# Optimization experiments

Hardware: AMD Instinct MI355X
Metric: run time of the kernel (lower is better)

The kernel has to match this reference:

```python
import jax, jax.numpy as jnp
import numpy as np
from jax import lax

PI = float(np.pi)
K_TOP = 128
N_BINS = 64

def _normalize(x, axis, eps=1e-12):
    n = jnp.sqrt(jnp.sum(x * x, axis=axis, keepdims=True))
    return x / jnp.maximum(n, eps)

def _conv(x, w, b):
    y = lax.conv_general_dilated(x, w, (1, 1), 'SAME',
                                 dimension_numbers=('NCHW', 'OIHW', 'NCHW'))
    return y + b[None, :, None, None]

def _maxpool2(x):
    return lax.reduce_window(x, -jnp.inf, lax.max, (1, 1, 2, 2), (1, 1, 2, 2), 'VALID')

def setup_inputs() -> dict:
    key = jax.random.key(0)
    ks = jax.random.split(key, 12)
    B, C, H, W = 16, 1, 512, 512
    PD, NPT = 128, 64
    fc_in = NPT + 64 * 4 * 4 + 3  # 1091
    def lin_init(k, fan_in, shape):
        bound = 1.0 / np.sqrt(fan_in)
        return jax.random.uniform(k, shape, jnp.float32, -bound, bound)
    return {
        'image': jax.random.normal(ks[0], (B, C, H, W), jnp.float32),
        'pattern_receptors': jax.random.normal(ks[1], (NPT, PD), jnp.float32) * 0.1,
        'conv1_w': lin_init(ks[2], 2 * 9, (32, 2, 3, 3)),
        'conv1_b': lin_init(ks[3], 2 * 9, (32,)),
        'conv2_w': lin_init(ks[4], 32 * 9, (64, 32, 3, 3)),
        'conv2_b': lin_init(ks[5], 32 * 9, (64,)),
        'fc1_w': lin_init(ks[6], fc_in, (512, fc_in)),
        'fc1_b': lin_init(ks[7], fc_in, (512,)),
        'fc2_w': lin_init(ks[8], 512, (PD, 512)),
        'fc2_b': lin_init(ks[9], 512, (PD,)),
        'ln_g': jnp.ones((PD,), jnp.float32),
        'ln_b': jnp.zeros((PD,), jnp.float32),
    }

def reference(image, pattern_receptors, conv1_w, conv1_b, conv2_w, conv2_b,
              fc1_w, fc1_b, fc2_w, fc2_b, ln_g, ln_b):
    B, C, H, W = image.shape
    # ---- frequency domain ----
    freq = jnp.fft.fft2(image, axes=(2, 3))
    magnitude = jnp.abs(freq)
    phase = jnp.angle(freq)
    # ---- pattern matching (topk of FFT magnitude vs receptor library) ----
    flat_mag = magnitude.reshape(B, C, -1)
    dom, _ = lax.top_k(flat_mag, K_TOP)          # [B, C, 128]
    dom = dom.reshape(B, -1)                     # [B, C*128]
    sims = jnp.matmul(_normalize(dom, 1), _normalize(pattern_receptors, 1).T)  # [B, 64]
    # ---- spatial path (original detaches via numpy roundtrip) ----
    img = lax.stop_gradient(image)
    gy = jnp.gradient(img, axis=2)
    gx = jnp.gradient(img, axis=3)
    gmag = jnp.sqrt(gx * gx + gy * gy)
    gori = jnp.arctan2(gy, gx)
    spat_in = jnp.stack([gmag, gori], axis=2).reshape(B, 2 * C, H, W)
    h = jax.nn.relu(_conv(spat_in, conv1_w, conv1_b))
    h = _maxpool2(h)                             # [B,32,H/2,W/2]
    h = jax.nn.relu(_conv(h, conv2_w, conv2_b))  # [B,64,H/2,W/2]
    Hp, Wp = h.shape[2], h.shape[3]
    h = h.reshape(B, 64, 4, Hp // 4, 4, Wp // 4).mean(axis=(3, 5))  # adaptive avg 4x4
    spatial = h.reshape(B, -1)                   # [B, 1024]
    # ---- phase statistics ----
    pf = phase.reshape(B, -1)
    p_mean = jnp.mean(pf, axis=1)
    p_std = jnp.std(pf, axis=1, ddof=1)
    bins = jnp.clip(jnp.floor((pf + PI) / (2 * PI) * N_BINS), 0, N_BINS - 1).astype(jnp.int32)
    hist = jnp.zeros((B, N_BINS), jnp.float32).at[jnp.arange(B)[:, None], bins].add(1.0)
    hist = hist / jnp.sum(hist, axis=1, keepdims=True)
    p_ent = -jnp.sum(hist * jnp.log(hist + 1e-10), axis=1)
    phase_feats = jnp.stack([p_mean, p_std, p_ent], axis=1)  # [B, 3]
    # ---- fuse: MLP + LayerNorm ----
    combined = jnp.concatenate([sims, spatial, phase_feats], axis=1)  # [B, 1091]
    z = jax.nn.relu(combined @ fc1_w.T + fc1_b)
    z = z @ fc2_w.T + fc2_b
    mu = jnp.mean(z, axis=-1, keepdims=True)
    var = jnp.var(z, axis=-1, keepdims=True)
    holo = (z - mu) / jnp.sqrt(var + 1e-5) * ln_g + ln_b
    return sims, spatial, phase_feats, holo
```

## Files before the change

### kernel.cpp

```cpp
#include <hip/hip_runtime.h>
#include <hip/hip_fp16.h>
#include <math.h>


#define PI_F 3.14159274f
#define TWO_PI_F 6.28318548f

typedef _Float16 half8 __attribute__((ext_vector_type(8)));
typedef _Float16 h2 __attribute__((ext_vector_type(2)));
typedef float floatx4 __attribute__((ext_vector_type(4)));

#define OFF_BIG   8388608
#define OFF_SMALL 25165824
#define NBIN 2048

__global__ void __launch_bounds__(256) init_kernel(float* __restrict__ zp,
                                                   float2* __restrict__ tw,
                                                   const float* __restrict__ w2,
                                                   const float* __restrict__ w1,
                                                   _Float16* __restrict__ wrep,
                                                   _Float16* __restrict__ w1r) {
    int idx = blockIdx.x * 256 + threadIdx.x;
    if (idx < 82992) zp[idx] = 0.0f;
    if (idx < 512) {
        if (idx == 0) tw[0] = make_float2(1.f, 0.f);
        else {
            int h = 31 - __clz(idx);
            int H = 1 << h;
            float sn, cs;
            sincosf(-PI_F * (float)(idx - H) / (float)H, &sn, &cs);
            tw[idx] = make_float2(cs, sn);
        }
    }
    if (idx < 18432) {
        int j = idx & 7;
        int lane = (idx >> 3) & 63;
        int nt = (idx >> 9) & 3;
        int tap = idx >> 11;
        int oc = nt * 16 + (lane & 15);
        int ic = (lane >> 4) * 8 + j;
        wrep[idx] = (_Float16)w2[(oc * 32 + ic) * 9 + tap];
    }
    if (idx < 1024) {
        int j = idx & 7;
        int lane = (idx >> 3) & 63;
        int nt = idx >> 9;
        int oc = 2 * (lane & 15) + nt;
        int k = (lane >> 4) * 8 + j;
        _Float16 v = (_Float16)0.f;
        if (k < 18) {
            int tap = k >> 1, ch = k & 1;
            v = (_Float16)w1[oc * 18 + ch * 9 + tap];
        }
        w1r[idx] = v;
    }
}

__global__ void __launch_bounds__(256) fft_rows2(const float* __restrict__ img,
                                                 const float2* __restrict__ twg,
                                                 h2* __restrict__ rowhf) {
    __shared__ float2 s[512];
    __shared__ float2 tw[512];
    const int t = threadIdx.x;
    const long long rbase = (long long)blockIdx.x * 1024;
    const float* x0 = img + rbase;
    const float* x1 = x0 + 512;

    for (int i = t; i < 512; i += 256) tw[i] = twg[i];
    for (int i = t; i < 512; i += 256) s[i] = make_float2(x0[i], x1[i]);
    __syncthreads();
#pragma unroll
    for (int st = 9; st >= 1; --st) {
        const int half = 1 << (st - 1);
        const int pos = t & (half - 1);
        const int grp = t >> (st - 1);
        const int i1 = (grp << st) + pos;
        const int i2 = i1 + half;
        float2 w = tw[half + pos];
        float2 a = s[i1], b = s[i2];
        float dx = a.x - b.x, dy = a.y - b.y;
        s[i1] = make_float2(a.x + b.x, a.y + b.y);
        s[i2] = make_float2(dx * w.x - dy * w.y, dx * w.y + dy * w.x);
        __syncthreads();
    }
    for (int i = t; i < 512; i += 256) {
        int k = __brev((unsigned)i) >> 23;
        int kp = (512 - k) & 511;
        int jp = __brev((unsigned)kp) >> 23;
        float2 Z = s[i], Zp = s[jp];
        rowhf[rbase + i]       = h2{(_Float16)(0.5f * (Z.x + Zp.x)),
                                    (_Float16)(0.5f * (Z.y - Zp.y))};
        rowhf[rbase + 512 + i] = h2{(_Float16)(0.5f * (Z.y + Zp.y)),
                                    (_Float16)(-0.5f * (Z.x - Zp.x))};
    }
}

#define FCOLS 16
__global__ void __launch_bounds__(512) fft_cols(const h2* __restrict__ rowhf,
                                                const float2* __restrict__ twg,
                                                _Float16* __restrict__ magT,
                                                float* __restrict__ psum,
                                                float* __restrict__ psumsq,
                                                unsigned* __restrict__ phist,
                                                unsigned* __restrict__ mhist) {
    __shared__ h2 sh[FCOLS * 512];
    __shared__ float2 tw[512];
    __shared__ unsigned ph[64];
    __shared__ unsigned mh[NBIN];
    __shared__ float red[16];
    const int t = threadIdx.x;
    const int b = blockIdx.x >> 5;
    const int x0 = (blockIdx.x & 31) * FCOLS;

    for (int i = t; i < 512; i += 512) tw[i] = twg[i];
    if (t < 64) ph[t] = 0u;
    for (int i = t; i < NBIN; i += 512) mh[i] = 0u;
    for (int idx = t; idx < FCOLS * 512; idx += 512) {
        int y = idx >> 4, c = idx & 15;
        sh[c * 512 + y] = rowhf[((size_t)(b * 512 + y)) * 512 + x0 + c];
    }
    __syncthreads();

    const int c = t >> 5;
    const int j = t & 31;
    float2 v[16];
#pragma unroll
    for (int r = 0; r < 16; ++r) {
        h2 hv = sh[c * 512 + j + 32 * r];
        v[r] = make_float2((float)hv[0], (float)hv[1]);
    }
#pragma unroll
    for (int r = 0; r < 8; ++r) {
        float2 w = tw[256 + j + 32 * r];
        float2 a = v[r], bb = v[r + 8];
        float dx = a.x - bb.x, dy = a.y - bb.y;
        v[r]     = make_float2(a.x + bb.x, a.y + bb.y);
        v[r + 8] = make_float2(dx * w.x - dy * w.y, dx * w.y + dy * w.x);
    }
#pragma unroll
    for (int g = 0; g < 2; ++g)
#pragma unroll
        for (int rr = 0; rr < 4; ++rr) {
            int r = g * 8 + rr;
            float2 w = tw[128 + j + 32 * rr];
            float2 a = v[r], bb = v[r + 4];
            float dx = a.x - bb.x, dy = a.y - bb.y;
            v[r]     = make_float2(a.x + bb.x, a.y + bb.y);
            v[r + 4] = make_float2(dx * w.x - dy * w.y, dx * w.y + dy * w.x);
        }
#pragma unroll
    for (int g = 0; g < 4; ++g)
#pragma unroll
        for (int rr = 0; rr < 2; ++rr) {
            int r = g * 4 + rr;
            float2 w = tw[64 + j + 32 * rr];
            float2 a = v[r], bb = v[r + 2];
            float dx = a.x - bb.x, dy = a.y - bb.y;
            v[r]     = make_float2(a.x + bb.x, a.y + bb.y);
            v[r + 2] = make_float2(dx * w.x - dy * w.y, dx * w.y + dy * w.x);
        }
    {
        float2 w = tw[32 + j];
#pragma unroll
        for (int g = 0; g < 8; ++g) {
            int r = g * 2;
            float2 a = v[r], bb = v[r + 1];
            float dx = a.x - bb.x, dy = a.y - bb.y;
            v[r]     = make_float2(a.x + bb.x, a.y + bb.y);
            v[r + 1] = make_float2(dx * w.x - dy * w.y, dx * w.y + dy * w.x);
        }
    }
#pragma unroll
    for (int hs = 4; hs >= 0; --hs) {
        const int h = 1 << hs;
        float2 w = tw[h + (j & (h - 1))];
        const bool upper = (j & h) != 0;
#pragma unroll
        for (int r = 0; r < 16; ++r) {
            float ox = __shfl_xor(v[r].x, h);
            float oy = __shfl_xor(v[r].y, h);
            float sx = v[r].x + ox, sy = v[r].y + oy;
            float dx = ox - v[r].x, dy = oy - v[r].y;
            float tx = dx * w.x - dy * w.y, ty = dx * w.y + dy * w.x;
            v[r].x = upper ? tx : sx;
            v[r].y = upper ? ty : sy;
        }
    }

    float lsum = 0.f, lsq = 0.f;
    _Float16* mcol = magT + ((size_t)(b * 512 + x0 + c)) * 512;
#pragma unroll
    for (int r = 0; r < 16; ++r) {
        float mag = sqrtf(v[r].x * v[r].x + v[r].y * v[r].y);
        union { _Float16 h; unsigned short u; } cvt;
        cvt.h = (_Float16)mag;
        mcol[j + 32 * r] = cvt.h;
        atomicAdd(&mh[min((unsigned)(cvt.u >> 4), (unsigned)(NBIN - 1))], 1u);
        float phv = atan2f(v[r].y, v[r].x);
        lsum += phv;
        lsq += phv * phv;
        int bin = min(max((int)floorf((phv + PI_F) / TWO_PI_F * 64.0f), 0), 63);
        atomicAdd(&ph[bin], 1u);
    }
    for (int off = 32; off > 0; off >>= 1) {
        lsum += __shfl_down(lsum, off);
        lsq  += __shfl_down(lsq, off);
    }
    if ((t & 63) == 0) { red[t >> 6] = lsum; red[8 + (t >> 6)] = lsq; }
    __syncthreads();
    if (t == 0) {
        float s = 0.f, q = 0.f;
        for (int i = 0; i < 8; ++i) { s += red[i]; q += red[8 + i]; }
        atomicAdd(psum + b, s);
        atomicAdd(psumsq + b, q);
    }
    if (t < 64 && ph[t]) atomicAdd(&phist[b * 64 + t], ph[t]);
    for (int i = t; i < NBIN; i += 512)
        if (mh[i]) atomicAdd(&mhist[b * NBIN + i], mh[i]);
}

__global__ void __launch_bounds__(256) thresh_kernel(const unsigned* __restrict__ mhist,
                                                     int* __restrict__ selbin) {
    __shared__ unsigned csum[256];
    const int b = blockIdx.x, t = threadIdx.x;
    unsigned s = 0;
    for (int i = 0; i < NBIN / 256; ++i) s += mhist[b * NBIN + t * (NBIN / 256) + i];
    csum[t] = s;
    __syncthreads();
    if (t == 0) {
        unsigned acc = 0; int chunk = 0;
        for (int i = 255; i >= 0; --i) {
            acc += csum[i];
            if (acc >= 128u) { chunk = i; break; }
        }
        unsigned acc2 = acc - csum[chunk];
        int tb = chunk * (NBIN / 256);
        for (int i = chunk * (NBIN / 256) + (NBIN / 256) - 1; i >= chunk * (NBIN / 256); --i) {
            acc2 += mhist[b * NBIN + i];
            if (acc2 >= 128u) { tb = i; break; }
        }
        selbin[b] = tb;
    }
}

#define TK_CAP 4096
__global__ void __launch_bounds__(256) collect_kernel(const _Float16* __restrict__ magT,
                                                      const int* __restrict__ selbin,
                                                      float* __restrict__ cand,
                                                      unsigned* __restrict__ ccnt) {
    const int blk = blockIdx.x;
    const int b = blk >> 4, chunk = blk & 15;
    const unsigned tb = (unsigned)selbin[b];
    const uint4* m = (const uint4*)(magT + (size_t)b * 262144 + chunk * 16384);
    float* cb = cand + b * TK_CAP;
    for (int i = threadIdx.x; i < 2048; i += 256) {
        uint4 v4 = m[i];
        unsigned vv[4] = {v4.x, v4.y, v4.z, v4.w};
#pragma unroll
        for (int j = 0; j < 4; ++j) {
#pragma unroll
            for (int k = 0; k < 2; ++k) {
                unsigned short ub = (k == 0) ? (unsigned short)(vv[j] & 0xFFFFu)
                                             : (unsigned short)(vv[j] >> 16);
                if ((unsigned)(ub >> 4) >= tb) {
                    unsigned p = atomicAdd(&ccnt[b], 1u);
                    if (p < TK_CAP) {
                        union { unsigned short u; _Float16 h; } c2;
                        c2.u = ub;
                        cb[p] = (float)c2.h;
                    }
                }
            }
        }
    }
}

__global__ void __launch_bounds__(1024) sort_kernel(const float* __restrict__ cand,
                                                    const unsigned* __restrict__ ccnt,
                                                    float* __restrict__ dom) {
    __shared__ float c[TK_CAP];
    const int b = blockIdx.x, t = threadIdx.x;
    const unsigned n = min(ccnt[b], (unsigned)TK_CAP);
    int P = 256;
    while (P < (int)n) P <<= 1;
    for (int i = t; i < P; i += 1024) c[i] = (i < (int)n) ? cand[b * TK_CAP + i] : -1.0f;
    __syncthreads();
    for (int k = 2; k <= P; k <<= 1) {
        for (int j = k >> 1; j > 0; j >>= 1) {
            for (int i = t; i < P; i += 1024) {
                int ixj = i ^ j;
                if (ixj > i) {
                    float a = c[i], d = c[ixj];
                    bool up = ((i & k) == 0);
                    if (up ? (a < d) : (a > d)) { c[i] = d; c[ixj] = a; }
                }
            }
            __syncthreads();
        }
    }
    if (t < 128) dom[b * 128 + t] = c[t];
}

__global__ void __launch_bounds__(256) sims_kernel(const float* __restrict__ dom,
                                                   const float* __restrict__ rec,
                                                   float* __restrict__ comb,
                                                   float* __restrict__ dout) {
    __shared__ float sd[16 * 128];
    __shared__ float sr[64 * 128];
    __shared__ float scale[80];
    const int t = threadIdx.x;
    for (int i = t; i < 2048; i += 256) sd[i] = dom[i];
    for (int i = t; i < 8192; i += 256) sr[i] = rec[i];
    __syncthreads();
    if (t < 80) {
        const float* base = (t < 16) ? (sd + t * 128) : (sr + (t - 16) * 128);
        float s = 0.f;
        for (int k = 0; k < 128; ++k) s += base[k] * base[k];
        scale[t] = 1.0f / fmaxf(sqrtf(s), 1e-12f);
    }
    __syncthreads();
    for (int o = t; o < 1024; o += 256) {
        int b = o >> 6, p = o & 63;
        const float* dv = sd + b * 128;
        const float* rv = sr + p * 128;
        float s = 0.f;
        for (int k = 0; k < 128; ++k) s += dv[k] * rv[k];
        float val = s * scale[b] * scale[16 + p];
        dout[b * 64 + p] = val;
        comb[b * 1091 + p] = val;
    }
}

__global__ void __launch_bounds__(256) grad_conv1_mfma(const float* __restrict__ img,
                                                       const half8* __restrict__ w1r,
                                                       const float* __restrict__ c1b,
                                                       _Float16* __restrict__ h1) {
    __shared__ float simg[36 * 37];
    __shared__ _Float16 sgrad[(34 * 36 + 1) * 2];
    const int blk = blockIdx.x;
    const int b = blk >> 8;
    const int tr = blk & 255;
    const int TY = (tr >> 4) * 32, TX = (tr & 15) * 32;
    const int t = threadIdx.x;
    const float* im = img + (long long)b * 262144;

    for (int idx = t; idx < 1296; idx += 256) {
        int iy = idx / 36, ix = idx - iy * 36;
        int gy = min(max(TY - 2 + iy, 0), 511);
        int gx = min(max(TX - 2 + ix, 0), 511);
        simg[iy * 37 + ix] = im[gy * 512 + gx];
    }
    if (t == 0) { sgrad[2448] = (_Float16)0.f; sgrad[2449] = (_Float16)0.f; }
    __syncthreads();

    for (int idx = t; idx < 1156; idx += 256) {
        int ly = idx / 34, lx = idx - ly * 34;
        int gy = TY - 1 + ly, gx = TX - 1 + lx;
        float up = simg[ly * 37 + lx + 1];
        float dn = simg[(ly + 2) * 37 + lx + 1];
        float lf = simg[(ly + 1) * 37 + lx];
        float rt = simg[(ly + 1) * 37 + lx + 2];
        float fy = (gy <= 0 || gy >= 511) ? 1.f : 0.5f;
        float fx = (gx <= 0 || gx >= 511) ? 1.f : 0.5f;
        float gyv = (dn - up) * fy, gxv = (rt - lf) * fx;
        bool inside = ((unsigned)gy < 512u) && ((unsigned)gx < 512u);
        float mag = inside ? sqrtf(gxv * gxv + gyv * gyv) : 0.f;
        float ori = inside ? atan2f(gyv, gxv) : 0.f;
        int p = (ly * 36 + lx) * 2;
        sgrad[p] = (_Float16)mag;
        sgrad[p + 1] = (_Float16)ori;
    }
    __syncthreads();

    const int w = t >> 6, lane = t & 63;
    const int q = lane >> 4, m = lane & 15;
    const int oc0 = 2 * m, oc1 = 2 * m + 1;
    const float bias0 = c1b[oc0], bias1 = c1b[oc1];
    half8 Bf0 = w1r[lane], Bf1 = w1r[64 + lane];
    const unsigned* gp = (const unsigned*)sgrad;
    const int ZP = 1224;

    const int sy = (m >> 1) & 1, sx = m & 1, dqx = m >> 2;

#pragma unroll 4
    for (int i = 0; i < 16; ++i) {
        const int mt = w * 16 + i;
        const int qy = mt >> 2, qxg = mt & 3;
        const int py = 2 * qy + sy;
        const int px = 2 * (qxg * 4 + dqx) + sx;
        const int base = py * 36 + px;

        int o0 = (q == 0) ? base      : (q == 1) ? base + 37 : (q == 2) ? base + 74 : ZP;
        int o1 = (q == 0) ? base + 1  : (q == 1) ? base + 38 : ZP;
        int o2 = (q == 0) ? base + 2  : (q == 1) ? base + 72 : ZP;
        int o3 = (q == 0) ? base + 36 : (q == 1) ? base + 73 : ZP;

        union { unsigned u[4]; half8 h; } Af;
        Af.u[0] = gp[o0]; Af.u[1] = gp[o1]; Af.u[2] = gp[o2]; Af.u[3] = gp[o3];

        floatx4 acc0 = {bias0, bias0, bias0, bias0};
        floatx4 acc1 = {bias1, bias1, bias1, bias1};
        acc0 = __builtin_amdgcn_mfma_f32_16x16x32_f16(Af.h, Bf0, acc0, 0, 0, 0);
        acc1 = __builtin_amdgcn_mfma_f32_16x16x32_f16(Af.h, Bf1, acc1, 0, 0, 0);

        float v0 = fmaxf(fmaxf(acc0[0], acc0[1]), fmaxf(acc0[2], acc0[3]));
        float v1 = fmaxf(fmaxf(acc1[0], acc1[1]), fmaxf(acc1[2], acc1[3]));
        v0 = fmaxf(v0, 0.f);
        v1 = fmaxf(v1, 0.f);

        const int PY = (TY >> 1) + qy;
        const int PX = (TX >> 1) + qxg * 4 + q;
        _Float16* dst = h1 + (((size_t)(b * 256 + PY)) * 256 + PX) * 32;
        *(h2*)(dst + oc0) = h2{(_Float16)v0, (_Float16)v1};
    }
}

__global__ void __launch_bounds__(256) conv2_mfma(const _Float16* __restrict__ h1,
                                                  const _Float16* __restrict__ wrep,
                                                  const float* __restrict__ c2b,
                                                  float* __restrict__ sacc) {
    __shared__ _Float16 tile[18 * 34 * 32];
    __shared__ float lsum[64];
    const int blk = blockIdx.x;
    const int b  = blk >> 7;
    const int yt = (blk >> 3) & 15;
    const int xt = blk & 7;
    const int y0 = yt * 16, x0 = xt * 32;
    const int t = threadIdx.x;
    if (t < 64) lsum[t] = 0.f;

    for (int c = t; c < 18 * 136; c += 256) {
        int row = c / 136;
        int chunk = c - row * 136;
        int gy = y0 - 1 + row;
        int px = chunk >> 2;
        int gx = x0 - 1 + px;
        floatx4 v = {0.f, 0.f, 0.f, 0.f};
        if ((unsigned)gy < 256u && (unsigned)gx < 256u)
            v = *(const floatx4*)(h1 + (((size_t)(b * 256 + gy)) * 256 + gx) * 32 + (chunk & 3) * 8);
        *(floatx4*)(tile + (row * 34 + px) * 32 + (chunk & 3) * 8) = v;
    }
    __syncthreads();

    const int w = t >> 6, lane = t & 63;
    const int q = lane >> 4, ln15 = lane & 15;
    float bias[4];
#pragma unroll
    for (int nt = 0; nt < 4; ++nt) bias[nt] = c2b[nt * 16 + ln15];
    float partial[4] = {0.f, 0.f, 0.f, 0.f};

#pragma unroll 1
    for (int gr = 0; gr < 2; ++gr) {
        floatx4 acc[4][4];
#pragma unroll
        for (int mt = 0; mt < 4; ++mt)
#pragma unroll
            for (int nt = 0; nt < 4; ++nt)
                acc[mt][nt] = floatx4{bias[nt], bias[nt], bias[nt], bias[nt]};

        const _Float16* ab = tile + (((w * 4 + gr * 2) * 34) + ln15) * 32 + q * 8;
        const _Float16* wk = wrep + lane * 8;

#pragma unroll 1
        for (int ky = 0; ky < 3; ++ky) {
#pragma unroll
            for (int kx = 0; kx < 3; ++kx) {
                half8 Bf[4];
#pragma unroll
                for (int nt = 0; nt < 4; ++nt)
                    Bf[nt] = *(const half8*)(wk + (kx * 4 + nt) * 512);
#pragma unroll
                for (int mt = 0; mt < 4; ++mt) {
                    half8 Af = *(const half8*)(ab + (mt >> 1) * 1088 + (mt & 1) * 512 + kx * 32);
#pragma unroll
                    for (int nt = 0; nt < 4; ++nt)
                        acc[mt][nt] = __builtin_amdgcn_mfma_f32_16x16x32_f16(Af, Bf[nt], acc[mt][nt], 0, 0, 0);
                }
            }
            ab += 34 * 32;
            wk += 3 * 2048;
        }

#pragma unroll
        for (int mt = 0; mt < 4; ++mt)
#pragma unroll
            for (int nt = 0; nt < 4; ++nt)
#pragma unroll
                for (int rg = 0; rg < 4; ++rg)
                    partial[nt] += fmaxf(acc[mt][nt][rg], 0.f);
    }

#pragma unroll
    for (int nt = 0; nt < 4; ++nt) {
        float v = partial[nt];
        v += __shfl_xor(v, 16);
        v += __shfl_xor(v, 32);
        if (lane < 16) atomicAdd(&lsum[nt * 16 + ln15], v);
    }
    __syncthreads();
    const int cell = (yt >> 2) * 4 + (xt >> 1);
    if (t < 64) atomicAdd(&sacc[(((b << 6) + t) << 4) + cell], lsum[t]);
}

__global__ void __launch_bounds__(256) finalize_kernel(const float* __restrict__ sacc,
                                                       const float* __restrict__ psum,
                                                       const float* __restrict__ psumsq,
                                                       const unsigned* __restrict__ phist,
                                                       float* __restrict__ comb,
                                                       float* __restrict__ dout) {
    if (blockIdx.x < 64) {
        int idx = blockIdx.x * 256 + threadIdx.x;
        int b = idx >> 10, j = idx & 1023;
        float v = sacc[idx] * (1.0f / 4096.0f);
        dout[1024 + idx] = v;
        comb[b * 1091 + 64 + j] = v;
    } else {
        int t = threadIdx.x;
        if (t < 16) {
            const float N = 262144.f;
            float s = psum[t];
            float mean = s / N;
            float var = (psumsq[t] - s * s / N) / (N - 1.f);
            float sd = sqrtf(fmaxf(var, 0.f));
            float ent = 0.f;
            for (int i = 0; i < 64; ++i) {
                float p = (float)phist[t * 64 + i] / N;
                ent -= p * logf(p + 1e-10f);
            }
            dout[17408 + t * 3 + 0] = mean;
            dout[17408 + t * 3 + 1] = sd;
            dout[17408 + t * 3 + 2] = ent;
            float* cb = comb + t * 1091 + 1088;
            cb[0] = mean; cb[1] = sd; cb[2] = ent;
        }
    }
}

__global__ void __launch_bounds__(256) fc1_kernel(const float* __restrict__ comb,
                                                  const float* __restrict__ W1,
                                                  const float* __restrict__ B1,
                                                  float* __restrict__ out1) {
    const int wid = blockIdx.x * 4 + (threadIdx.x >> 6);
    const int lane = threadIdx.x & 63;
    const int b = wid >> 9, o = wid & 511;
    const float* w = W1 + (size_t)o * 1091;
    const float* c = comb + b * 1091;
    float acc = 0.f;
#pragma unroll 4
    for (int i = 0; i < 17; ++i) {
        int k = i * 64 + lane;
        acc += w[k] * c[k];
    }
    if (lane < 3) acc += w[1088 + lane] * c[1088 + lane];
#pragma unroll
    for (int off = 32; off > 0; off >>= 1) acc += __shfl_down(acc, off);
    if (lane == 0) out1[b * 512 + o] = fmaxf(acc + B1[o], 0.f);
}

__global__ void __launch_bounds__(256) fc2_kernel(const float* __restrict__ out1,
                                                  const float* __restrict__ W2,
                                                  const float* __restrict__ B2,
                                                  float* __restrict__ z) {
    const int wid = blockIdx.x * 4 + (threadIdx.x >> 6);
    const int lane = threadIdx.x & 63;
    const int b = wid >> 7, o = wid & 127;
    const float* w = W2 + (size_t)o * 512;
    const float* c = out1 + b * 512;
    float acc = 0.f;
#pragma unroll
    for (int i = 0; i < 8; ++i) {
        int k = i * 64 + lane;
        acc += w[k] * c[k];
    }
#pragma unroll
    for (int off = 32; off > 0; off >>= 1) acc += __shfl_down(acc, off);
    if (lane == 0) z[b * 128 + o] = acc + B2[o];
}

__global__ void __launch_bounds__(128) ln_kernel(const float* __restrict__ z,
                                                 const float* __restrict__ g,
                                                 const float* __restrict__ beta,
                                                 float* __restrict__ dout) {
    __shared__ float red[4];
    const int b = blockIdx.x, t = threadIdx.x;
    float acc = z[b * 128 + t];
    float s = acc;
    for (int off = 32; off > 0; off >>= 1) s += __shfl_down(s, off);
    if ((t & 63) == 0) red[t >> 6] = s;
    __syncthreads();
    float mu = (red[0] + red[1]) * (1.0f / 128.0f);
    float d = acc - mu;
    float q = d * d;
    for (int off = 32; off > 0; off >>= 1) q += __shfl_down(q, off);
    if ((t & 63) == 0) red[2 + (t >> 6)] = q;
    __syncthreads();
    float var = (red[2] + red[3]) * (1.0f / 128.0f);
    dout[17456 + b * 128 + t] = d / sqrtf(var + 1e-5f) * g[t] + beta[t];
}

extern "C" void kernel_launch(void* const* d_in, const int* in_sizes, int n_in,
                              void* d_out, int out_size, void* d_ws, size_t ws_size,
                              hipStream_t stream) {
    const float* img = (const float*)d_in[0];
    const float* rec = (const float*)d_in[1];
    const float* w1  = (const float*)d_in[2];
    const float* c1b = (const float*)d_in[3];
    const float* w2  = (const float*)d_in[4];
    const float* c2b = (const float*)d_in[5];
    const float* fw1 = (const float*)d_in[6];
    const float* fb1 = (const float*)d_in[7];
    const float* fw2 = (const float*)d_in[8];
    const float* fb2 = (const float*)d_in[9];
    const float* lng = (const float*)d_in[10];
    const float* lnb = (const float*)d_in[11];
    float* out = (float*)d_out;

    float* ws = (float*)d_ws;
    h2* rowhf       = (h2*)ws;
    _Float16* magT  = (_Float16*)(ws + OFF_BIG);
    _Float16* h1    = (_Float16*)(ws + OFF_BIG);
    float* small_  = ws + OFF_SMALL;
    float* sacc    = small_;
    float* psum    = small_ + 16384;
    float* psumsq  = small_ + 16400;
    unsigned* phist = (unsigned*)(small_ + 16416);
    unsigned* mhist = (unsigned*)(small_ + 17440);
    unsigned* ccnt  = (unsigned*)(small_ + 82976);
    int* selbin    = (int*)(small_ + 82992);
    float* dom     = small_ + 83008;
    float* comb    = small_ + 85056;
    float* out1    = small_ + 102512;
    _Float16* wrep = (_Float16*)(small_ + 110704);
    float2* twg    = (float2*)(small_ + 119920);
    float* cand    = small_ + 120944;
    float* zbuf    = cand;
    _Float16* w1r  = (_Float16*)(small_ + 186480);

    init_kernel<<<325, 256, 0, stream>>>(sacc, twg, w2, w1, wrep, w1r);
    fft_rows2<<<4096, 256, 0, stream>>>(img, twg, rowhf);
    fft_cols<<<512, 512, 0, stream>>>(rowhf, twg, magT, psum, psumsq, phist, mhist);
    thresh_kernel<<<16, 256, 0, stream>>>(mhist, selbin);
    collect_kernel<<<256, 256, 0, stream>>>(magT, selbin, cand, ccnt);
    sort_kernel<<<16, 1024, 0, stream>>>(cand, ccnt, dom);
    sims_kernel<<<1, 256, 0, stream>>>(dom, rec, comb, out);
    grad_conv1_mfma<<<4096, 256, 0, stream>>>(img, (const half8*)w1r, c1b, h1);
    conv2_mfma<<<2048, 256, 0, stream>>>(h1, wrep, c2b, sacc);
    finalize_kernel<<<65, 256, 0, stream>>>(sacc, psum, psumsq, phist, comb, out);
    fc1_kernel<<<2048, 256, 0, stream>>>(comb, fw1, fb1, out1);
    fc2_kernel<<<512, 256, 0, stream>>>(out1, fw2, fb2, zbuf);
    ln_kernel<<<16, 128, 0, stream>>>(zbuf, lng, lnb, out);
}
```

Measured before the change: 279.5 us.

## Fuse column FFT, top-k threshold and candidate collection into cooperative kernel

Replaces the column-FFT, threshold and collect kernels with one cooperative kernel of 256 blocks. Each block processes 32 columns and keeps the fp16 magnitudes in registers. After a grid-wide sync it finds the threshold bin with a shared-memory suffix scan and collects candidates directly, so the magnitude array is never written to or re-read from global memory. The similarity computation moves into the sort kernel, removing a single-block launch. In exchange, each block does two column passes serially, and the grid barrier plus the fixed 256-block grid may limit occupancy.

```diff
diff --git a/kernel.cpp b/kernel.cpp
--- a/kernel.cpp
+++ b/kernel.cpp
@@ -1,6 +1,9 @@
 #include <hip/hip_runtime.h>
 #include <hip/hip_fp16.h>
+#include <hip/hip_cooperative_groups.h>
 #include <math.h>
+
+namespace cg = cooperative_groups;
 
 
 #define PI_F 3.14159274f
@@ -95,113 +98,128 @@
     }
 }
 
-#define FCOLS 16
-__global__ void __launch_bounds__(512) fft_cols(const h2* __restrict__ rowhf,
-                                                const float2* __restrict__ twg,
-                                                _Float16* __restrict__ magT,
-                                                float* __restrict__ psum,
-                                                float* __restrict__ psumsq,
-                                                unsigned* __restrict__ phist,
-                                                unsigned* __restrict__ mhist) {
-    __shared__ h2 sh[FCOLS * 512];
+#define TK_CAP 4096
+__global__ void __launch_bounds__(512) fftcol_coop(const h2* __restrict__ rowhf,
+                                                   const float2* __restrict__ twg,
+                                                   float* __restrict__ psum,
+                                                   float* __restrict__ psumsq,
+                                                   unsigned* __restrict__ phist,
+                                                   unsigned* __restrict__ mhist,
+                                                   float* __restrict__ cand,
+                                                   unsigned* __restrict__ ccnt) {
+    __shared__ h2 sh[16 * 512];
     __shared__ float2 tw[512];
     __shared__ unsigned ph[64];
     __shared__ unsigned mh[NBIN];
     __shared__ float red[16];
+    __shared__ unsigned scanA[512], scanB[512];
+    __shared__ int seltb;
     const int t = threadIdx.x;
-    const int b = blockIdx.x >> 5;
-    const int x0 = (blockIdx.x & 31) * FCOLS;
+    const int b = blockIdx.x >> 4;
+    const int xg = blockIdx.x & 15;
 
     for (int i = t; i < 512; i += 512) tw[i] = twg[i];
     if (t < 64) ph[t] = 0u;
     for (int i = t; i < NBIN; i += 512) mh[i] = 0u;
-    for (int idx = t; idx < FCOLS * 512; idx += 512) {
-        int y = idx >> 4, c = idx & 15;
-        sh[c * 512 + y] = rowhf[((size_t)(b * 512 + y)) * 512 + x0 + c];
-    }
-    __syncthreads();
 
     const int c = t >> 5;
     const int j = t & 31;
-    float2 v[16];
-#pragma unroll
-    for (int r = 0; r < 16; ++r) {
-        h2 hv = sh[c * 512 + j + 32 * r];
-        v[r] = make_float2((float)hv[0], (float)hv[1]);
-    }
-#pragma unroll
-    for (int r = 0; r < 8; ++r) {
-        float2 w = tw[256 + j + 32 * r];
-        float2 a = v[r], bb = v[r + 8];
-        float dx = a.x - bb.x, dy = a.y - bb.y;
-        v[r]     = make_float2(a.x + bb.x, a.y + bb.y);
-        v[r + 8] = make_float2(dx * w.x - dy * w.y, dx * w.y + dy * w.x);
-    }
-#pragma unroll
-    for (int g = 0; g < 2; ++g)
-#pragma unroll
-        for (int rr = 0; rr < 4; ++rr) {
-            int r = g * 8 + rr;
-            float2 w = tw[128 + j + 32 * rr];
-            float2 a = v[r], bb = v[r + 4];
+    float lsum = 0.f, lsq = 0.f;
+    unsigned mgp[16];
+
+#pragma unroll 1
+    for (int cgi = 0; cgi < 2; ++cgi) {
+        const int x0 = xg * 32 + cgi * 16;
+        __syncthreads();
+        for (int idx = t; idx < 16 * 512; idx += 512) {
+            int y = idx >> 4, cc = idx & 15;
+            sh[cc * 512 + y] = rowhf[((size_t)(b * 512 + y)) * 512 + x0 + cc];
+        }
+        __syncthreads();
+
+        float2 v[16];
+#pragma unroll
+        for (int r = 0; r < 16; ++r) {
+            h2 hv = sh[c * 512 + j + 32 * r];
+            v[r] = make_float2((float)hv[0], (float)hv[1]);
+        }
+        __syncthreads();
+
+#pragma unroll
+        for (int r = 0; r < 8; ++r) {
+            float2 w = tw[256 + j + 32 * r];
+            float2 a = v[r], bb = v[r + 8];
             float dx = a.x - bb.x, dy = a.y - bb.y;
             v[r]     = make_float2(a.x + bb.x, a.y + bb.y);
-            v[r + 4] = make_float2(dx * w.x - dy * w.y, dx * w.y + dy * w.x);
-        }
-#pragma unroll
-    for (int g = 0; g < 4; ++g)
-#pragma unroll
-        for (int rr = 0; rr < 2; ++rr) {
-            int r = g * 4 + rr;
-            float2 w = tw[64 + j + 32 * rr];
-            float2 a = v[r], bb = v[r + 2];
-            float dx = a.x - bb.x, dy = a.y - bb.y;
-            v[r]     = make_float2(a.x + bb.x, a.y + bb.y);
-            v[r + 2] = make_float2(dx * w.x - dy * w.y, dx * w.y + dy * w.x);
-        }
-    {
-        float2 w = tw[32 + j];
-#pragma unroll
-        for (int g = 0; g < 8; ++g) {
-            int r = g * 2;
-            float2 a = v[r], bb = v[r + 1];
-            float dx = a.x - bb.x, dy = a.y - bb.y;
-            v[r]     = make_float2(a.x + bb.x, a.y + bb.y);
-            v[r + 1] = make_float2(dx * w.x - dy * w.y, dx * w.y + dy * w.x);
-        }
-    }
-#pragma unroll
-    for (int hs = 4; hs >= 0; --hs) {
-        const int h = 1 << hs;
-        float2 w = tw[h + (j & (h - 1))];
-        const bool upper = (j & h) != 0;
+            v[r + 8] = make_float2(dx * w.x - dy * w.y, dx * w.y + dy * w.x);
+        }
+#pragma unroll
+        for (int g = 0; g < 2; ++g)
+#pragma unroll
+            for (int rr = 0; rr < 4; ++rr) {
+                int r = g * 8 + rr;
+                float2 w = tw[128 + j + 32 * rr];
+                float2 a = v[r], bb = v[r + 4];
+                float dx = a.x - bb.x, dy = a.y - bb.y;
+                v[r]     = make_float2(a.x + bb.x, a.y + bb.y);
+                v[r + 4] = make_float2(dx * w.x - dy * w.y, dx * w.y + dy * w.x);
+            }
+#pragma unroll
+        for (int g = 0; g < 4; ++g)
+#pragma unroll
+            for (int rr = 0; rr < 2; ++rr) {
+                int r = g * 4 + rr;
+                float2 w = tw[64 + j + 32 * rr];
+                float2 a = v[r], bb = v[r + 2];
+                float dx = a.x - bb.x, dy = a.y - bb.y;
+                v[r]     = make_float2(a.x + bb.x, a.y + bb.y);
+                v[r + 2] = make_float2(dx * w.x - dy * w.y, dx * w.y + dy * w.x);
+            }
+        {
+            float2 w = tw[32 + j];
+#pragma unroll
+            for (int g = 0; g < 8; ++g) {
+                int r = g * 2;
+                float2 a = v[r], bb = v[r + 1];
+                float dx = a.x - bb.x, dy = a.y - bb.y;
+                v[r]     = make_float2(a.x + bb.x, a.y + bb.y);
+                v[r + 1] = make_float2(dx * w.x - dy * w.y, dx * w.y + dy * w.x);
+            }
+        }
+#pragma unroll
+        for (int hs = 4; hs >= 0; --hs) {
+            const int h = 1 << hs;
+            float2 w = tw[h + (j & (h - 1))];
+            const bool upper = (j & h) != 0;
+#pragma unroll
+            for (int r = 0; r < 16; ++r) {
+                float ox = __shfl_xor(v[r].x, h);
+                float oy = __shfl_xor(v[r].y, h);
+                float sx = v[r].x + ox, sy = v[r].y + oy;
+                float dx = ox - v[r].x, dy = oy - v[r].y;
+                float tx = dx * w.x - dy * w.y, ty = dx * w.y + dy * w.x;
+                v[r].x = upper ? tx : sx;
+                v[r].y = upper ? ty : sy;
+            }
+        }
+
 #pragma unroll
         for (int r = 0; r < 16; ++r) {
-            float ox = __shfl_xor(v[r].x, h);
-            float oy = __shfl_xor(v[r].y, h);
-            float sx = v[r].x + ox, sy = v[r].y + oy;
-            float dx = ox - v[r].x, dy = oy - v[r].y;
-            float tx = dx * w.x - dy * w.y, ty = dx * w.y + dy * w.x;
-            v[r].x = upper ? tx : sx;
-            v[r].y = upper ? ty : sy;
-        }
-    }
-
-    float lsum = 0.f, lsq = 0.f;
-    _Float16* mcol = magT + ((size_t)(b * 512 + x0 + c)) * 512;
-#pragma unroll
-    for (int r = 0; r < 16; ++r) {
-        float mag = sqrtf(v[r].x * v[r].x + v[r].y * v[r].y);
-        union { _Float16 h; unsigned short u; } cvt;
-        cvt.h = (_Float16)mag;
-        mcol[j + 32 * r] = cvt.h;
-        atomicAdd(&mh[min((unsigned)(cvt.u >> 4), (unsigned)(NBIN - 1))], 1u);
-        float phv = atan2f(v[r].y, v[r].x);
-        lsum += phv;
-        lsq += phv * phv;
-        int bin = min(max((int)floorf((phv + PI_F) / TWO_PI_F * 64.0f), 0), 63);
-        atomicAdd(&ph[bin], 1u);
-    }
+            float mag = sqrtf(v[r].x * v[r].x + v[r].y * v[r].y);
+            union { _Float16 h; unsigned short u; } cvt;
+            cvt.h = (_Float16)mag;
+            int ei = cgi * 16 + r;
+            if (ei & 1) mgp[ei >> 1] |= ((unsigned)cvt.u) << 16;
+            else        mgp[ei >> 1] = (unsigned)cvt.u;
+            atomicAdd(&mh[min((unsigned)(cvt.u >> 4), (unsigned)(NBIN - 1))], 1u);
+            float phv = atan2f(v[r].y, v[r].x);
+            lsum += phv;
+            lsq += phv * phv;
+            int bin = min(max((int)floorf((phv + PI_F) / TWO_PI_F * 64.0f), 0), 63);
+            atomicAdd(&ph[bin], 1u);
+        }
+    }
+
     for (int off = 32; off > 0; off >>= 1) {
         lsum += __shfl_down(lsum, off);
         lsq  += __shfl_down(lsq, off);
@@ -217,58 +235,53 @@
     if (t < 64 && ph[t]) atomicAdd(&phist[b * 64 + t], ph[t]);
     for (int i = t; i < NBIN; i += 512)
         if (mh[i]) atomicAdd(&mhist[b * NBIN + i], mh[i]);
-}
-
-__global__ void __launch_bounds__(256) thresh_kernel(const unsigned* __restrict__ mhist,
-                                                     int* __restrict__ selbin) {
-    __shared__ unsigned csum[256];
-    const int b = blockIdx.x, t = threadIdx.x;
-    unsigned s = 0;
-    for (int i = 0; i < NBIN / 256; ++i) s += mhist[b * NBIN + t * (NBIN / 256) + i];
-    csum[t] = s;
-    __syncthreads();
-    if (t == 0) {
-        unsigned acc = 0; int chunk = 0;
-        for (int i = 255; i >= 0; --i) {
-            acc += csum[i];
-            if (acc >= 128u) { chunk = i; break; }
-        }
-        unsigned acc2 = acc - csum[chunk];
-        int tb = chunk * (NBIN / 256);
-        for (int i = chunk * (NBIN / 256) + (NBIN / 256) - 1; i >= chunk * (NBIN / 256); --i) {
-            acc2 += mhist[b * NBIN + i];
-            if (acc2 >= 128u) { tb = i; break; }
-        }
-        selbin[b] = tb;
-    }
-}
-
-#define TK_CAP 4096
-__global__ void __launch_bounds__(256) collect_kernel(const _Float16* __restrict__ magT,
-                                                      const int* __restrict__ selbin,
-                                                      float* __restrict__ cand,
-                                                      unsigned* __restrict__ ccnt) {
-    const int blk = blockIdx.x;
-    const int b = blk >> 4, chunk = blk & 15;
-    const unsigned tb = (unsigned)selbin[b];
-    const uint4* m = (const uint4*)(magT + (size_t)b * 262144 + chunk * 16384);
+
+    cg::this_grid().sync();
+
+    {
+        unsigned s = 0;
+#pragma unroll
+        for (int i = 0; i < 4; ++i) s += mhist[b * NBIN + t * 4 + i];
+        scanA[t] = s;
+        __syncthreads();
+        unsigned* src = scanA;
+        unsigned* dst = scanB;
+#pragma unroll
+        for (int off = 1; off < 512; off <<= 1) {
+            unsigned val = src[t] + ((t + off < 512) ? src[t + off] : 0u);
+            dst[t] = val;
+            __syncthreads();
+            unsigned* tmp = src; src = dst; dst = tmp;
+            __syncthreads();
+        }
+        unsigned sufNext = (t < 511) ? src[t + 1] : 0u;
+        if (src[t] >= 128u && sufNext < 128u) {
+            unsigned acc = sufNext;
+            int tb = t * 4;
+            for (int i = t * 4 + 3; i >= t * 4; --i) {
+                acc += mhist[b * NBIN + i];
+                if (acc >= 128u) { tb = i; break; }
+            }
+            seltb = tb;
+        }
+        __syncthreads();
+    }
+    const unsigned tb = (unsigned)seltb;
+
     float* cb = cand + b * TK_CAP;
-    for (int i = threadIdx.x; i < 2048; i += 256) {
-        uint4 v4 = m[i];
-        unsigned vv[4] = {v4.x, v4.y, v4.z, v4.w};
-#pragma unroll
-        for (int j = 0; j < 4; ++j) {
-#pragma unroll
-            for (int k = 0; k < 2; ++k) {
-                unsigned short ub = (k == 0) ? (unsigned short)(vv[j] & 0xFFFFu)
-                                             : (unsigned short)(vv[j] >> 16);
-                if ((unsigned)(ub >> 4) >= tb) {
-                    unsigned p = atomicAdd(&ccnt[b], 1u);
-                    if (p < TK_CAP) {
-                        union { unsigned short u; _Float16 h; } c2;
-                        c2.u = ub;
-                        cb[p] = (float)c2.h;
-                    }
+#pragma unroll
+    for (int i = 0; i < 16; ++i) {
+        unsigned vv = mgp[i];
+#pragma unroll
+        for (int k = 0; k < 2; ++k) {
+            unsigned short ub = (k == 0) ? (unsigned short)(vv & 0xFFFFu)
+                                         : (unsigned short)(vv >> 16);
+            if ((unsigned)(ub >> 4) >= tb) {
+                unsigned p = atomicAdd(&ccnt[b], 1u);
+                if (p < TK_CAP) {
+                    union { unsigned short u; _Float16 h; } c2;
+                    c2.u = ub;
+                    cb[p] = (float)c2.h;
                 }
             }
         }
@@ -277,7 +290,9 @@
 
 __global__ void __launch_bounds__(1024) sort_kernel(const float* __restrict__ cand,
                                                     const unsigned* __restrict__ ccnt,
-                                                    float* __restrict__ dom) {
+                                                    const float* __restrict__ rec,
+                                                    float* __restrict__ comb,
+                                                    float* __restrict__ dout) {
     __shared__ float c[TK_CAP];
     const int b = blockIdx.x, t = threadIdx.x;
     const unsigned n = min(ccnt[b], (unsigned)TK_CAP);
@@ -298,36 +313,19 @@
             __syncthreads();
         }
     }
-    if (t < 128) dom[b * 128 + t] = c[t];
-}
-
-__global__ void __launch_bounds__(256) sims_kernel(const float* __restrict__ dom,
-                                                   const float* __restrict__ rec,
-                                                   float* __restrict__ comb,
-                                                   float* __restrict__ dout) {
-    __shared__ float sd[16 * 128];
-    __shared__ float sr[64 * 128];
-    __shared__ float scale[80];
-    const int t = threadIdx.x;
-    for (int i = t; i < 2048; i += 256) sd[i] = dom[i];
-    for (int i = t; i < 8192; i += 256) sr[i] = rec[i];
-    __syncthreads();
-    if (t < 80) {
-        const float* base = (t < 16) ? (sd + t * 128) : (sr + (t - 16) * 128);
-        float s = 0.f;
-        for (int k = 0; k < 128; ++k) s += base[k] * base[k];
-        scale[t] = 1.0f / fmaxf(sqrtf(s), 1e-12f);
-    }
-    __syncthreads();
-    for (int o = t; o < 1024; o += 256) {
-        int b = o >> 6, p = o & 63;
-        const float* dv = sd + b * 128;
-        const float* rv = sr + p * 128;
-        float s = 0.f;
-        for (int k = 0; k < 128; ++k) s += dv[k] * rv[k];
-        float val = s * scale[b] * scale[16 + p];
-        dout[b * 64 + p] = val;
-        comb[b * 1091 + p] = val;
+    if (t < 64) {
+        float dn = 0.f;
+        for (int k = 0; k < 128; ++k) dn += c[k] * c[k];
+        const float* rv = rec + t * 128;
+        float rn = 0.f, dot = 0.f;
+        for (int k = 0; k < 128; ++k) {
+            float r = rv[k];
+            rn += r * r;
+            dot += c[k] * r;
+        }
+        float val = dot / (fmaxf(sqrtf(dn), 1e-12f) * fmaxf(sqrtf(rn), 1e-12f));
+        dout[b * 64 + t] = val;
+        comb[b * 1091 + t] = val;
     }
 }
 
@@ -374,8 +372,8 @@
 
     const int w = t >> 6, lane = t & 63;
     const int q = lane >> 4, m = lane & 15;
-    const int oc0 = 2 * m, oc1 = 2 * m + 1;
-    const float bias0 = c1b[oc0], bias1 = c1b[oc1];
+    const int oc0 = 2 * m;
+    const float bias0 = c1b[oc0], bias1 = c1b[oc0 + 1];
     half8 Bf0 = w1r[lane], Bf1 = w1r[64 + lane];
     const unsigned* gp = (const unsigned*)sgrad;
     const int ZP = 1224;
@@ -617,7 +615,6 @@
 
     float* ws = (float*)d_ws;
     h2* rowhf       = (h2*)ws;
-    _Float16* magT  = (_Float16*)(ws + OFF_BIG);
     _Float16* h1    = (_Float16*)(ws + OFF_BIG);
     float* small_  = ws + OFF_SMALL;
     float* sacc    = small_;
@@ -626,8 +623,6 @@
     unsigned* phist = (unsigned*)(small_ + 16416);
     unsigned* mhist = (unsigned*)(small_ + 17440);
     unsigned* ccnt  = (unsigned*)(small_ + 82976);
-    int* selbin    = (int*)(small_ + 82992);
-    float* dom     = small_ + 83008;
     float* comb    = small_ + 85056;
     float* out1    = small_ + 102512;
     _Float16* wrep = (_Float16*)(small_ + 110704);
@@ -638,11 +633,15 @@
 
     init_kernel<<<325, 256, 0, stream>>>(sacc, twg, w2, w1, wrep, w1r);
     fft_rows2<<<4096, 256, 0, stream>>>(img, twg, rowhf);
-    fft_cols<<<512, 512, 0, stream>>>(rowhf, twg, magT, psum, psumsq, phist, mhist);
-    thresh_kernel<<<16, 256, 0, stream>>>(mhist, selbin);
-    collect_kernel<<<256, 256, 0, stream>>>(magT, selbin, cand, ccnt);
-    sort_kernel<<<16, 1024, 0, stream>>>(cand, ccnt, dom);
-    sims_kernel<<<1, 256, 0, stream>>>(dom, rec, comb, out);
+    {
+        const h2* rp = rowhf;
+        const float2* tp = twg;
+        void* cargs[] = { (void*)&rp, (void*)&tp, (void*)&psum, (void*)&psumsq,
+                          (void*)&phist, (void*)&mhist, (void*)&cand, (void*)&ccnt };
+        hipLaunchCooperativeKernel((const void*)fftcol_coop, dim3(256), dim3(512),
+                                   cargs, 0, stream);
+    }
+    sort_kernel<<<16, 1024, 0, stream>>>(cand, ccnt, rec, comb, out);
     grad_conv1_mfma<<<4096, 256, 0, stream>>>(img, (const half8*)w1r, c1b, h1);
     conv2_mfma<<<2048, 256, 0, stream>>>(h1, wrep, c2b, sacc);
     finalize_kernel<<<65, 256, 0, stream>>>(sacc, psum, psumsq, phist, comb, out);
```

Result: slower. 325.9 us (+16.6%).
